# Optimization experiments

Hardware: AMD Instinct MI355X
Metric: run time of the kernel (lower is better)

Reference implementation:

```python
import jax, jax.numpy as jnp
import numpy as np

BN_EPS = 1e-5


def conv3x3(x, w, b):
    # x: [B,C,H,W], w: [O,C,3,3], same padding, stride 1
    y = jax.lax.conv_general_dilated(x, w, (1, 1), ((1, 1), (1, 1)),
                                     dimension_numbers=('NCHW', 'OIHW', 'NCHW'))
    return y + b[None, :, None, None]


def bilinear_sample(x, py, px):
    # x: [B,C,H,W]; py/px: [B,K,H,W] fractional sample coords (zero outside borders)
    B, C, H, W = x.shape
    y0 = jnp.floor(py)
    x0 = jnp.floor(px)
    wy1 = py - y0  # frac weights
    wx1 = px - x0

    def corner(yc, xc, wgt):
        valid = (yc >= 0) & (yc <= H - 1) & (xc >= 0) & (xc <= W - 1)
        yi = jnp.clip(yc, 0, H - 1).astype(jnp.int32)
        xi = jnp.clip(xc, 0, W - 1).astype(jnp.int32)
        # gather per batch: [C,H,W] indexed by [K,H,W] -> [C,K,H,W]
        g = jax.vmap(lambda img, yy, xx: img[:, yy, xx])(x, yi, xi)  # [B,C,K,H,W]
        return g * jnp.where(valid, wgt, 0.0)[:, None]

    return (corner(y0, x0, (1 - wy1) * (1 - wx1))
            + corner(y0, x0 + 1, (1 - wy1) * wx1)
            + corner(y0 + 1, x0, wy1 * (1 - wx1))
            + corner(y0 + 1, x0 + 1, wy1 * wx1))  # [B,C,9,H,W]


def deform_conv(x, conv_w, off_w, off_b, mask_w, mask_b, gamma, beta):
    B, C, H, W = x.shape
    O = conv_w.shape[0]
    offset = conv3x3(x, off_w, off_b)                      # [B,18,H,W]
    mask = jax.nn.sigmoid(conv3x3(x, mask_w, mask_b))      # [B,9,H,W]
    off = offset.reshape(B, 9, 2, H, W)                    # tap k = kh*3+kw, (dy,dx)
    ky = jnp.repeat(jnp.arange(3), 3).astype(x.dtype)      # kernel row per tap
    kx = jnp.tile(jnp.arange(3), 3).astype(x.dtype)        # kernel col per tap
    gy = jnp.arange(H, dtype=x.dtype)
    gx = jnp.arange(W, dtype=x.dtype)
    # sample position = out pos - pad + kernel idx + learned offset
    py = off[:, :, 0] + gy[None, None, :, None] + (ky - 1.0)[None, :, None, None]
    px = off[:, :, 1] + gx[None, None, None, :] + (kx - 1.0)[None, :, None, None]
    val = bilinear_sample(x, py, px)                       # [B,C,9,H,W]
    val = val * mask[:, None]                              # modulated (DCNv2)
    out = jnp.einsum('bckhw,ock->bohw', val, conv_w.reshape(O, C, 9))
    # BatchNorm (training-mode batch stats) + ReLU
    mean = out.mean(axis=(0, 2, 3))
    var = out.var(axis=(0, 2, 3))
    out = (out - mean[None, :, None, None]) * jax.lax.rsqrt(var + BN_EPS)[None, :, None, None]
    out = out * gamma[None, :, None, None] + beta[None, :, None, None]
    return jax.nn.relu(out)


def setup_inputs() -> dict:
    key = jax.random.key(0)
    ks = jax.random.split(key, 8)
    B, Cin, Cout, H, W = 2, 64, 64, 128, 128
    x = jax.random.normal(ks[0], (B, Cin, H, W), dtype=jnp.float32)
    fan = Cin * 9
    conv_w = jax.random.normal(ks[1], (Cout, Cin, 3, 3), dtype=jnp.float32) / np.sqrt(fan)
    # offset/mask convs: small random weights so offsets are non-degenerate but modest
    off_w = jax.random.normal(ks[2], (18, Cin, 3, 3), dtype=jnp.float32) * 0.01
    off_b = jax.random.normal(ks[3], (18,), dtype=jnp.float32) * 0.1
    mask_w = jax.random.normal(ks[4], (9, Cin, 3, 3), dtype=jnp.float32) * 0.01
    mask_b = jnp.zeros((9,), dtype=jnp.float32)
    gamma = jnp.ones((Cout,), dtype=jnp.float32)
    beta = jnp.zeros((Cout,), dtype=jnp.float32)
    return {"x": x, "conv_w": conv_w, "off_w": off_w, "off_b": off_b,
            "mask_w": mask_w, "mask_b": mask_b, "gamma": gamma, "beta": beta}


def reference(x, conv_w, off_w, off_b, mask_w, mask_b, gamma, beta):
    return deform_conv(x, conv_w, off_w, off_b, mask_w, mask_b, gamma, beta)
```

## Files before the change

### kernel.cpp

```cpp
#include <hip/hip_runtime.h>
#include <hip/hip_fp16.h>

typedef __attribute__((ext_vector_type(8))) _Float16 f16x8;
typedef __attribute__((ext_vector_type(4))) float f32x4;
typedef __attribute__((ext_vector_type(4))) unsigned int u32x4;
typedef unsigned int  u32;
typedef unsigned short u16;

constexpr int B_  = 2;
constexpr int C_  = 64;
constexpr int O_  = 64;
constexpr int H_  = 128;
constexpr int W_  = 128;
constexpr int HW_ = H_ * W_;
constexpr int NPIX_ = B_ * HW_;
constexpr float BN_EPS_ = 1e-5f;

constexpr int WROWS_ = 7;
constexpr int WCOLS_ = 70;
constexpr int WPIX_  = WROWS_ * WCOLS_;
constexpr int WSTR_  = 72;

__device__ __align__(16) u16   g_xt[(size_t)B_ * HW_ * 64];
__device__ __align__(16) u16   g_pre16[(size_t)B_ * O_ * HW_];
__device__ __align__(16) u16   g_WpF[36864];
__device__ __align__(16) u16   g_W27F[18432];
__device__ __align__(16) float g_part[262144];
__device__ __align__(16) float g_stats[128];

__device__ __forceinline__ u32 segsw(u32 px) { return ((px >> 3) & 3u) << 3; }

__device__ __forceinline__ u16 f2bf(float f) {
    u32 u = __float_as_uint(f);
    u = (u + 0x7fffu + ((u >> 16) & 1u)) >> 16;
    return (u16)u;
}
__device__ __forceinline__ float bflo(u32 u) { return __uint_as_float(u << 16); }
__device__ __forceinline__ float bfhi(u32 u) { return __uint_as_float(u & 0xffff0000u); }
__device__ __forceinline__ u16 f2h(float f) { return __half_as_ushort(__float2half(f)); }

__global__ __launch_bounds__(256)
void prep_kernel(const float* __restrict__ x, const float* __restrict__ conv_w,
                 const float* __restrict__ off_w, const float* __restrict__ mask_w) {
    int bid = blockIdx.x, tid = threadIdx.x;
    if (bid < 512) {
        __shared__ u16 tile[64][66];
        int b = bid >> 8;
        int hw0 = (bid & 255) * 64;
        int c = tid >> 2, pq = (tid & 3) * 16;
        const float* src = x + (((size_t)(b * 64 + c)) << 14) + hw0 + pq;
#pragma unroll
        for (int i = 0; i < 4; i++) {
            float4 v = *(const float4*)(src + i * 4);
            tile[pq + i * 4 + 0][c] = f2h(v.x);
            tile[pq + i * 4 + 1][c] = f2h(v.y);
            tile[pq + i * 4 + 2][c] = f2h(v.z);
            tile[pq + i * 4 + 3][c] = f2h(v.w);
        }
        __syncthreads();
        int p = tid >> 2, cs = (tid & 3) * 16;
        uint4* dst = (uint4*)(g_xt + (((size_t)(b << 14)) + hw0 + p) * 64 + cs);
        dst[0] = *(const uint4*)&tile[p][cs];
        dst[1] = *(const uint4*)&tile[p][cs + 8];
    } else if (bid < 512 + 144) {
        int i = (bid - 512) * 256 + tid;
        int j = i & 7, lane = (i >> 3) & 63, t = (i >> 9) & 3, s = i >> 11;
        int o = t * 16 + (lane & 15);
        int kk = s * 32 + (lane >> 4) * 8 + j;
        int tap = kk >> 6, c = kk & 63;
        g_WpF[i] = f2h(conv_w[(o * 64 + c) * 9 + tap]);
    } else {
        int i = (bid - 656) * 256 + tid;
        int j = i & 7, lane = (i >> 3) & 63, t = (i >> 9) & 1, s = i >> 10;
        int row = t * 16 + (lane & 15);
        int kk = s * 32 + (lane >> 4) * 8 + j;
        int tap = kk >> 6, c = kk & 63;
        float v = 0.f;
        if (row < 18) v = off_w[(row * 64 + c) * 9 + tap];
        else if (row < 27) v = mask_w[((row - 18) * 64 + c) * 9 + tap];
        g_W27F[i] = f2h(v);
    }
}

__device__ __forceinline__ void mfma4h(int lane, int sg, const f16x8& sv,
                                       f32x4 (&acc)[4]) {
#pragma unroll
    for (int t = 0; t < 4; t++) {
        f16x8 af = *(const f16x8*)(g_WpF + (u32)((sg * 4 + t) * 64 + lane) * 8u);
        acc[t] = __builtin_amdgcn_mfma_f32_16x16x32_f16(af, sv, acc[t], 0, 0, 0);
    }
}

__device__ __forceinline__ void metaBrt(const float* __restrict__ moff,
                                        const float* __restrict__ mmask,
                                        int tap, int p64, int h, int w, int cb,
                                        u32 qoff, u32* qc, u32* cwp) {
    float dy = moff[(2 * tap) * 64 + p64];
    float dx = moff[(2 * tap + 1) * 64 + p64];
    float m  = mmask[tap * 64 + p64];
    float kdy = (float)(tap / 3 - 1), kdx = (float)(tap % 3 - 1);
    float py = dy + (float)h + kdy;
    float px = dx + (float)w + kdx;
    float y0 = floorf(py), x0 = floorf(px);
    float ly = py - y0, lx = px - x0, hy = 1.f - ly, hx = 1.f - lx;
    float y1 = y0 + 1.f, x1 = x0 + 1.f;
    bool vy0 = (y0 >= 0.f) && (y0 <= 127.f);
    bool vy1 = (y1 >= 0.f) && (y1 <= 127.f);
    bool vx0 = (x0 >= 0.f) && (x0 <= 127.f);
    bool vx1 = (x1 >= 0.f) && (x1 <= 127.f);
    int iy0 = (int)fminf(fmaxf(y0, 0.f), 127.f);
    int iy1 = (int)fminf(fmaxf(y1, 0.f), 127.f);
    int ix0 = (int)fminf(fmaxf(x0, 0.f), 127.f);
    int ix1 = (int)fminf(fmaxf(x1, 0.f), 127.f);
    int w00 = min(max(iy0 * WCOLS_ + ix0 - cb, 0), WPIX_ - 1);
    int w01 = min(max(iy0 * WCOLS_ + ix1 - cb, 0), WPIX_ - 1);
    int w10 = min(max(iy1 * WCOLS_ + ix0 - cb, 0), WPIX_ - 1);
    int w11 = min(max(iy1 * WCOLS_ + ix1 - cb, 0), WPIX_ - 1);
    qc[0] = (u32)w00 * WSTR_ + (qoff ^ segsw((u32)w00));
    qc[1] = (u32)w01 * WSTR_ + (qoff ^ segsw((u32)w01));
    qc[2] = (u32)w10 * WSTR_ + (qoff ^ segsw((u32)w10));
    qc[3] = (u32)w11 * WSTR_ + (qoff ^ segsw((u32)w11));
    __half2 c0 = __float2half2_rn((vy0 && vx0) ? hy * hx * m : 0.f);
    __half2 c1 = __float2half2_rn((vy0 && vx1) ? hy * lx * m : 0.f);
    __half2 c2 = __float2half2_rn((vy1 && vx0) ? ly * hx * m : 0.f);
    __half2 c3 = __float2half2_rn((vy1 && vx1) ? ly * lx * m : 0.f);
    cwp[0] = *(const u32*)&c0; cwp[1] = *(const u32*)&c1;
    cwp[2] = *(const u32*)&c2; cwp[3] = *(const u32*)&c3;
}

__device__ __forceinline__ void ld4(const u16* __restrict__ win, const u32* qc,
                                    u32 sc, uint4* p) {
#pragma unroll
    for (int i = 0; i < 4; i++) p[i] = *(const uint4*)(win + qc[i] + sc);
}

__device__ __forceinline__ f16x8 cmbH(const uint4* p, const u32* cwp) {
    const u32* a = &p[0].x; const u32* b = &p[1].x;
    const u32* c = &p[2].x; const u32* d = &p[3].x;
    __half2 cw0 = *(const __half2*)&cwp[0], cw1 = *(const __half2*)&cwp[1];
    __half2 cw2 = *(const __half2*)&cwp[2], cw3 = *(const __half2*)&cwp[3];
    u32x4 r;
#pragma unroll
    for (int i = 0; i < 4; i++) {
        __half2 t = __hmul2(*(const __half2*)&a[i], cw0);
        t = __hfma2(*(const __half2*)&b[i], cw1, t);
        t = __hfma2(*(const __half2*)&c[i], cw2, t);
        t = __hfma2(*(const __half2*)&d[i], cw3, t);
        r[i] = *(const u32*)&t;
    }
    return __builtin_bit_cast(f16x8, r);
}

template<int OS>
__device__ __forceinline__ void phaseB(const u16* __restrict__ win,
                                       const float* __restrict__ moff,
                                       const float* __restrict__ mmask,
                                       int p64, int h, int w, int cb,
                                       u32 qoff, int lane, f32x4 (&acc)[4]) {
    u32 q[4]; u32 cw[4];
#pragma unroll
    for (int ls = 0; ls < 9; ls++) {
        const int s   = OS * 9 + ls;
        const int tap = s >> 1;
        const int kh  = s & 1;
        if (kh == 0 || ls == 0)
            metaBrt(moff, mmask, tap, p64, h, w, cb, qoff, q, cw);
        uint4 p[4];
        ld4(win, q, (u32)(kh * 32), p);
        f16x8 sv = cmbH(p, cw);
        mfma4h(lane, s, sv, acc);
    }
}

__global__ __launch_bounds__(512, 4)
void gemm_ab_kernel(const float* __restrict__ off_b, const float* __restrict__ mask_b) {
    __shared__ __align__(16) u16 win[(WPIX_ + 1) * WSTR_];
    __shared__ float moff[18 * 64];
    __shared__ float mmask[9 * 64];
    const int tid = threadIdx.x;
    const int lane = tid & 63, wv = tid >> 6;
    const int quad = lane >> 4, r = lane & 15;
    const int wp = wv & 3, os = wv >> 2;
    const int blk = (blockIdx.x & 7) * 64 + (blockIdx.x >> 3);
    const int pbase = blk * 64;
    const int b = pbase >> 14, hwb = pbase & (HW_ - 1);
    const int h = hwb >> 7, w0 = hwb & (W_ - 1);
    const int p64 = wp * 16 + r;
    const int w = w0 + p64;
    const int cb = (h - 3) * WCOLS_ + (w0 - 3);
    const u32 bb = (u32)b << 14;
    const u32 qoff = (u32)quad * 8u;

#pragma unroll
    for (int it = 0; it < 8; it++) {
        int i = tid + it * 512;
        if (i < WPIX_ * 8) {
            int px = i >> 3, seg = i & 7;
            int wr = px / WCOLS_, wc = px - wr * WCOLS_;
            int row = min(max(h - 3 + wr, 0), H_ - 1);
            int col = min(max(w0 - 3 + wc, 0), W_ - 1);
            u32 g = (bb + (u32)(row * W_ + col)) * 64u + (u32)seg * 8u;
            u32 d = (u32)px * WSTR_ + (((u32)seg * 8u) ^ segsw((u32)px));
            *(uint4*)(&win[d]) = *(const uint4*)(g_xt + g);
        } else if (i < WPIX_ * 8 + 8) {
            int seg = i - WPIX_ * 8;
            u32 d = (u32)WPIX_ * WSTR_ + (((u32)seg * 8u) ^ segsw((u32)WPIX_));
            *(uint4*)(&win[d]) = make_uint4(0, 0, 0, 0);
        }
    }
    __syncthreads();

    {
        u32 aq[9];
#pragma unroll
        for (int tap = 0; tap < 9; tap++) {
            int dh = tap / 3 - 1, dw = tap % 3 - 1;
            int hh = h + dh, ww = w + dw;
            bool valid = (hh >= 0) && (hh < H_) && (ww >= 0) && (ww < W_);
            u32 widx = valid ? (u32)((3 + dh) * WCOLS_ + (p64 + 3 + dw)) : (u32)WPIX_;
            aq[tap] = widx * WSTR_ + (qoff ^ segsw(widx));
        }
        f32x4 accA = (f32x4){0.f, 0.f, 0.f, 0.f};
        f16x8 ab[3];
        ab[0] = *(const f16x8*)(win + aq[0]);
        ab[1] = *(const f16x8*)(win + aq[0] + 32);
        ab[2] = *(const f16x8*)(win + aq[1]);
#pragma unroll
        for (int s = 0; s < 18; s++) {
            f16x8 sv = ab[s % 3];
            if (s + 3 < 18)
                ab[s % 3] = *(const f16x8*)(win + aq[(s + 3) >> 1] + ((s + 3) & 1) * 32);
            f16x8 af = *(const f16x8*)(g_W27F + (u32)((s * 2 + os) * 64 + lane) * 8u);
            accA = __builtin_amdgcn_mfma_f32_16x16x32_f16(af, sv, accA, 0, 0, 0);
        }
#pragma unroll
        for (int g = 0; g < 4; g++) {
            int o = os * 16 + quad * 4 + g;
            float v = accA[g];
            if (o < 18) {
                moff[o * 64 + p64] = v + off_b[o];
            } else if (o < 27) {
                v += mask_b[o - 18];
                mmask[(o - 18) * 64 + p64] = 1.f / (1.f + __expf(-v));
            }
        }
    }
    __syncthreads();

    f32x4 acc[4];
#pragma unroll
    for (int t = 0; t < 4; t++) acc[t] = (f32x4){0.f, 0.f, 0.f, 0.f};

    if (os == 0)
        phaseB<0>(win, moff, mmask, p64, h, w, cb, qoff, lane, acc);
    else
        phaseB<1>(win, moff, mmask, p64, h, w, cb, qoff, lane, acc);
    __syncthreads();

    float* ex = (float*)win;
    const u32 exi = (u32)p64 * 68u + (((u32)quad << 2) ^ ((((u32)p64 >> 3) & 3u) << 2));
    if (os == 1) {
#pragma unroll
        for (int t = 0; t < 4; t++)
            *(f32x4*)(ex + exi + (u32)t * 16u) = acc[t];
    }
    __syncthreads();

    if (os == 0) {
#pragma unroll
        for (int t = 0; t < 4; t++)
            acc[t] += *(const f32x4*)(ex + exi + (u32)t * 16u);

        const int hw = hwb + p64;
        const u32 slot = (u32)(blk * 4 + wp);
#pragma unroll
        for (int t = 0; t < 4; t++) {
#pragma unroll
            for (int g = 0; g < 4; g++) {
                float v = acc[t][g];
                int o = t * 16 + quad * 4 + g;
                g_pre16[(u32)(b * 64 + o) * HW_ + hw] = f2bf(v);
                float s = v, s2 = v * v;
#pragma unroll
                for (int off = 8; off >= 1; off >>= 1) {
                    s  += __shfl_down(s, off, 16);
                    s2 += __shfl_down(s2, off, 16);
                }
                if (r == 0) {
                    g_part[(u32)o * 2048 + slot] = s;
                    g_part[131072 + (u32)o * 2048 + slot] = s2;
                }
            }
        }
    }
}

__global__ __launch_bounds__(256)
void stats_red_kernel() {
    __shared__ float p4[4];
    int i = blockIdx.x;
    const float* src = g_part + (u32)(i >> 6) * 131072 + (u32)(i & 63) * 2048;
    float s = 0.f;
    for (int rr = threadIdx.x; rr < 2048; rr += 256) s += src[rr];
#pragma unroll
    for (int off = 32; off >= 1; off >>= 1) s += __shfl_down(s, off);
    if ((threadIdx.x & 63) == 0) p4[threadIdx.x >> 6] = s;
    __syncthreads();
    if (threadIdx.x == 0) g_stats[i] = p4[0] + p4[1] + p4[2] + p4[3];
}

__global__ __launch_bounds__(256)
void bn_relu_kernel(const float* __restrict__ gamma, const float* __restrict__ beta,
                    float* __restrict__ out) {
    int i4 = blockIdx.x * 256 + threadIdx.x;
    int ch = (i4 >> 12) & (O_ - 1);
    float mean = g_stats[ch] * (1.f / NPIX_);
    float var  = g_stats[64 + ch] * (1.f / NPIX_) - mean * mean;
    float scale = gamma[ch] * rsqrtf(var + BN_EPS_);
    float shift = beta[ch] - mean * scale;
    uint2 v = ((const uint2*)g_pre16)[i4];
    float4 o;
    o.x = fmaxf(fmaf(bflo(v.x), scale, shift), 0.f);
    o.y = fmaxf(fmaf(bfhi(v.x), scale, shift), 0.f);
    o.z = fmaxf(fmaf(bflo(v.y), scale, shift), 0.f);
    o.w = fmaxf(fmaf(bfhi(v.y), scale, shift), 0.f);
    ((float4*)out)[i4] = o;
}

extern "C" void kernel_launch(void* const* d_in, const int* in_sizes, int n_in,
                              void* d_out, int out_size, void* d_ws, size_t ws_size,
                              hipStream_t stream) {
    const float* x      = (const float*)d_in[0];
    const float* conv_w = (const float*)d_in[1];
    const float* off_w  = (const float*)d_in[2];
    const float* off_b  = (const float*)d_in[3];
    const float* mask_w = (const float*)d_in[4];
    const float* mask_b = (const float*)d_in[5];
    const float* gamma  = (const float*)d_in[6];
    const float* beta   = (const float*)d_in[7];
    float* out = (float*)d_out;
    (void)d_ws; (void)ws_size;

    prep_kernel<<<728, 256, 0, stream>>>(x, conv_w, off_w, mask_w);
    gemm_ab_kernel<<<NPIX_ / 64, 512, 0, stream>>>(off_b, mask_b);
    stats_red_kernel<<<128, 256, 0, stream>>>();
    bn_relu_kernel<<<2048, 256, 0, stream>>>(gamma, beta, out);
}
```

Baseline: 98.58 us.

## Read input directly from global memory instead of staging LDS window, halve block size

Removes the shared-memory halo window of channel-last input and has both the offset/mask conv and the bilinear gathers read g_xt directly from global (L1/L2), using a zero pixel appended at the end for padding. It also drops the two-wave-group split over taps and the LDS cross-group reduction, so each wave handles all 18 K-steps with 256 threads per block. This removes the window fill, several barriers and LDS pressure, which should allow more resident blocks. In exchange, the gathers become scattered global loads with cache-dependent latency, and each wave does twice the serial MFMA work.

```diff
diff --git a/kernel.cpp b/kernel.cpp
--- a/kernel.cpp
+++ b/kernel.cpp
@@ -16,19 +16,12 @@
 constexpr int NPIX_ = B_ * HW_;
 constexpr float BN_EPS_ = 1e-5f;
 
-constexpr int WROWS_ = 7;
-constexpr int WCOLS_ = 70;
-constexpr int WPIX_  = WROWS_ * WCOLS_;
-constexpr int WSTR_  = 72;
-
-__device__ __align__(16) u16   g_xt[(size_t)B_ * HW_ * 64];
+__device__ __align__(16) u16   g_xt[((size_t)NPIX_ + 1) * 64];
 __device__ __align__(16) u16   g_pre16[(size_t)B_ * O_ * HW_];
 __device__ __align__(16) u16   g_WpF[36864];
 __device__ __align__(16) u16   g_W27F[18432];
 __device__ __align__(16) float g_part[262144];
 __device__ __align__(16) float g_stats[128];
-
-__device__ __forceinline__ u32 segsw(u32 px) { return ((px >> 3) & 3u) << 3; }
 
 __device__ __forceinline__ u16 f2bf(float f) {
     u32 u = __float_as_uint(f);
@@ -79,6 +72,7 @@
         if (row < 18) v = off_w[(row * 64 + c) * 9 + tap];
         else if (row < 27) v = mask_w[((row - 18) * 64 + c) * 9 + tap];
         g_W27F[i] = f2h(v);
+        if (bid == 656 && tid < 64) g_xt[(size_t)NPIX_ * 64 + tid] = 0;
     }
 }
 
@@ -91,10 +85,10 @@
     }
 }
 
-__device__ __forceinline__ void metaBrt(const float* __restrict__ moff,
-                                        const float* __restrict__ mmask,
-                                        int tap, int p64, int h, int w, int cb,
-                                        u32 qoff, u32* qc, u32* cwp) {
+__device__ __forceinline__ void metaBrtG(const float* __restrict__ moff,
+                                         const float* __restrict__ mmask,
+                                         int tap, int p64, int h, int w, u32 bb,
+                                         u32 qoff, u32* qc, u32* cwp) {
     float dy = moff[(2 * tap) * 64 + p64];
     float dx = moff[(2 * tap + 1) * 64 + p64];
     float m  = mmask[tap * 64 + p64];
@@ -112,14 +106,10 @@
     int iy1 = (int)fminf(fmaxf(y1, 0.f), 127.f);
     int ix0 = (int)fminf(fmaxf(x0, 0.f), 127.f);
     int ix1 = (int)fminf(fmaxf(x1, 0.f), 127.f);
-    int w00 = min(max(iy0 * WCOLS_ + ix0 - cb, 0), WPIX_ - 1);
-    int w01 = min(max(iy0 * WCOLS_ + ix1 - cb, 0), WPIX_ - 1);
-    int w10 = min(max(iy1 * WCOLS_ + ix0 - cb, 0), WPIX_ - 1);
-    int w11 = min(max(iy1 * WCOLS_ + ix1 - cb, 0), WPIX_ - 1);
-    qc[0] = (u32)w00 * WSTR_ + (qoff ^ segsw((u32)w00));
-    qc[1] = (u32)w01 * WSTR_ + (qoff ^ segsw((u32)w01));
-    qc[2] = (u32)w10 * WSTR_ + (qoff ^ segsw((u32)w10));
-    qc[3] = (u32)w11 * WSTR_ + (qoff ^ segsw((u32)w11));
+    qc[0] = (bb + (u32)(iy0 * W_ + ix0)) * 64u + qoff;
+    qc[1] = (bb + (u32)(iy0 * W_ + ix1)) * 64u + qoff;
+    qc[2] = (bb + (u32)(iy1 * W_ + ix0)) * 64u + qoff;
+    qc[3] = (bb + (u32)(iy1 * W_ + ix1)) * 64u + qoff;
     __half2 c0 = __float2half2_rn((vy0 && vx0) ? hy * hx * m : 0.f);
     __half2 c1 = __float2half2_rn((vy0 && vx1) ? hy * lx * m : 0.f);
     __half2 c2 = __float2half2_rn((vy1 && vx0) ? ly * hx * m : 0.f);
@@ -128,10 +118,9 @@
     cwp[2] = *(const u32*)&c2; cwp[3] = *(const u32*)&c3;
 }
 
-__device__ __forceinline__ void ld4(const u16* __restrict__ win, const u32* qc,
-                                    u32 sc, uint4* p) {
-#pragma unroll
-    for (int i = 0; i < 4; i++) p[i] = *(const uint4*)(win + qc[i] + sc);
+__device__ __forceinline__ void ld4g(const u32* qc, u32 sc, uint4* p) {
+#pragma unroll
+    for (int i = 0; i < 4; i++) p[i] = *(const uint4*)(g_xt + qc[i] + sc);
 }
 
 __device__ __forceinline__ f16x8 cmbH(const uint4* p, const u32* cwp) {
@@ -151,64 +140,21 @@
     return __builtin_bit_cast(f16x8, r);
 }
 
-template<int OS>
-__device__ __forceinline__ void phaseB(const u16* __restrict__ win,
-                                       const float* __restrict__ moff,
-                                       const float* __restrict__ mmask,
-                                       int p64, int h, int w, int cb,
-                                       u32 qoff, int lane, f32x4 (&acc)[4]) {
-    u32 q[4]; u32 cw[4];
-#pragma unroll
-    for (int ls = 0; ls < 9; ls++) {
-        const int s   = OS * 9 + ls;
-        const int tap = s >> 1;
-        const int kh  = s & 1;
-        if (kh == 0 || ls == 0)
-            metaBrt(moff, mmask, tap, p64, h, w, cb, qoff, q, cw);
-        uint4 p[4];
-        ld4(win, q, (u32)(kh * 32), p);
-        f16x8 sv = cmbH(p, cw);
-        mfma4h(lane, s, sv, acc);
-    }
-}
-
-__global__ __launch_bounds__(512, 4)
+__global__ __launch_bounds__(256, 4)
 void gemm_ab_kernel(const float* __restrict__ off_b, const float* __restrict__ mask_b) {
-    __shared__ __align__(16) u16 win[(WPIX_ + 1) * WSTR_];
     __shared__ float moff[18 * 64];
     __shared__ float mmask[9 * 64];
     const int tid = threadIdx.x;
     const int lane = tid & 63, wv = tid >> 6;
     const int quad = lane >> 4, r = lane & 15;
-    const int wp = wv & 3, os = wv >> 2;
     const int blk = (blockIdx.x & 7) * 64 + (blockIdx.x >> 3);
     const int pbase = blk * 64;
     const int b = pbase >> 14, hwb = pbase & (HW_ - 1);
     const int h = hwb >> 7, w0 = hwb & (W_ - 1);
-    const int p64 = wp * 16 + r;
+    const int p64 = wv * 16 + r;
     const int w = w0 + p64;
-    const int cb = (h - 3) * WCOLS_ + (w0 - 3);
     const u32 bb = (u32)b << 14;
     const u32 qoff = (u32)quad * 8u;
-
-#pragma unroll
-    for (int it = 0; it < 8; it++) {
-        int i = tid + it * 512;
-        if (i < WPIX_ * 8) {
-            int px = i >> 3, seg = i & 7;
-            int wr = px / WCOLS_, wc = px - wr * WCOLS_;
-            int row = min(max(h - 3 + wr, 0), H_ - 1);
-            int col = min(max(w0 - 3 + wc, 0), W_ - 1);
-            u32 g = (bb + (u32)(row * W_ + col)) * 64u + (u32)seg * 8u;
-            u32 d = (u32)px * WSTR_ + (((u32)seg * 8u) ^ segsw((u32)px));
-            *(uint4*)(&win[d]) = *(const uint4*)(g_xt + g);
-        } else if (i < WPIX_ * 8 + 8) {
-            int seg = i - WPIX_ * 8;
-            u32 d = (u32)WPIX_ * WSTR_ + (((u32)seg * 8u) ^ segsw((u32)WPIX_));
-            *(uint4*)(&win[d]) = make_uint4(0, 0, 0, 0);
-        }
-    }
-    __syncthreads();
 
     {
         u32 aq[9];
@@ -217,79 +163,84 @@
             int dh = tap / 3 - 1, dw = tap % 3 - 1;
             int hh = h + dh, ww = w + dw;
             bool valid = (hh >= 0) && (hh < H_) && (ww >= 0) && (ww < W_);
-            u32 widx = valid ? (u32)((3 + dh) * WCOLS_ + (p64 + 3 + dw)) : (u32)WPIX_;
-            aq[tap] = widx * WSTR_ + (qoff ^ segsw(widx));
-        }
-        f32x4 accA = (f32x4){0.f, 0.f, 0.f, 0.f};
+            u32 pix = valid ? (bb + (u32)(hh * W_ + ww)) : (u32)NPIX_;
+            aq[tap] = pix * 64u + qoff;
+        }
+        f32x4 accA[2];
+        accA[0] = (f32x4){0.f, 0.f, 0.f, 0.f};
+        accA[1] = (f32x4){0.f, 0.f, 0.f, 0.f};
         f16x8 ab[3];
-        ab[0] = *(const f16x8*)(win + aq[0]);
-        ab[1] = *(const f16x8*)(win + aq[0] + 32);
-        ab[2] = *(const f16x8*)(win + aq[1]);
+        ab[0] = *(const f16x8*)(g_xt + aq[0]);
+        ab[1] = *(const f16x8*)(g_xt + aq[0] + 32);
+        ab[2] = *(const f16x8*)(g_xt + aq[1]);
 #pragma unroll
         for (int s = 0; s < 18; s++) {
             f16x8 sv = ab[s % 3];
             if (s + 3 < 18)
-                ab[s % 3] = *(const f16x8*)(win + aq[(s + 3) >> 1] + ((s + 3) & 1) * 32);
-            f16x8 af = *(const f16x8*)(g_W27F + (u32)((s * 2 + os) * 64 + lane) * 8u);
-            accA = __builtin_amdgcn_mfma_f32_16x16x32_f16(af, sv, accA, 0, 0, 0);
-        }
+                ab[s % 3] = *(const f16x8*)(g_xt + aq[(s + 3) >> 1] + ((s + 3) & 1) * 32);
+#pragma unroll
+            for (int t = 0; t < 2; t++) {
+                f16x8 af = *(const f16x8*)(g_W27F + (u32)((s * 2 + t) * 64 + lane) * 8u);
+                accA[t] = __builtin_amdgcn_mfma_f32_16x16x32_f16(af, sv, accA[t], 0, 0, 0);
+            }
+        }
+#pragma unroll
+        for (int t = 0; t < 2; t++) {
+#pragma unroll
+            for (int g = 0; g < 4; g++) {
+                int o = t * 16 + quad * 4 + g;
+                float v = accA[t][g];
+                if (o < 18) {
+                    moff[o * 64 + p64] = v + off_b[o];
+                } else if (o < 27) {
+                    v += mask_b[o - 18];
+                    mmask[(o - 18) * 64 + p64] = 1.f / (1.f + __expf(-v));
+                }
+            }
+        }
+    }
+
+    f32x4 acc[4];
+#pragma unroll
+    for (int t = 0; t < 4; t++) acc[t] = (f32x4){0.f, 0.f, 0.f, 0.f};
+    {
+        u32 q[4]; u32 cw[4];
+#pragma unroll
+        for (int tap = 0; tap < 9; tap++) {
+            metaBrtG(moff, mmask, tap, p64, h, w, bb, qoff, q, cw);
+            {
+                uint4 p0[4];
+                ld4g(q, 0, p0);
+                f16x8 sv = cmbH(p0, cw);
+                mfma4h(lane, tap * 2 + 0, sv, acc);
+            }
+            {
+                uint4 p1[4];
+                ld4g(q, 32, p1);
+                f16x8 sv = cmbH(p1, cw);
+                mfma4h(lane, tap * 2 + 1, sv, acc);
+            }
+        }
+    }
+
+    const int hw = hwb + p64;
+    const u32 slot = (u32)(blk * 4 + wv);
+#pragma unroll
+    for (int t = 0; t < 4; t++) {
 #pragma unroll
         for (int g = 0; g < 4; g++) {
-            int o = os * 16 + quad * 4 + g;
-            float v = accA[g];
-            if (o < 18) {
-                moff[o * 64 + p64] = v + off_b[o];
-            } else if (o < 27) {
-                v += mask_b[o - 18];
-                mmask[(o - 18) * 64 + p64] = 1.f / (1.f + __expf(-v));
-            }
-        }
-    }
-    __syncthreads();
-
-    f32x4 acc[4];
-#pragma unroll
-    for (int t = 0; t < 4; t++) acc[t] = (f32x4){0.f, 0.f, 0.f, 0.f};
-
-    if (os == 0)
-        phaseB<0>(win, moff, mmask, p64, h, w, cb, qoff, lane, acc);
-    else
-        phaseB<1>(win, moff, mmask, p64, h, w, cb, qoff, lane, acc);
-    __syncthreads();
-
-    float* ex = (float*)win;
-    const u32 exi = (u32)p64 * 68u + (((u32)quad << 2) ^ ((((u32)p64 >> 3) & 3u) << 2));
-    if (os == 1) {
-#pragma unroll
-        for (int t = 0; t < 4; t++)
-            *(f32x4*)(ex + exi + (u32)t * 16u) = acc[t];
-    }
-    __syncthreads();
-
-    if (os == 0) {
-#pragma unroll
-        for (int t = 0; t < 4; t++)
-            acc[t] += *(const f32x4*)(ex + exi + (u32)t * 16u);
-
-        const int hw = hwb + p64;
-        const u32 slot = (u32)(blk * 4 + wp);
-#pragma unroll
-        for (int t = 0; t < 4; t++) {
-#pragma unroll
-            for (int g = 0; g < 4; g++) {
-                float v = acc[t][g];
-                int o = t * 16 + quad * 4 + g;
-                g_pre16[(u32)(b * 64 + o) * HW_ + hw] = f2bf(v);
-                float s = v, s2 = v * v;
-#pragma unroll
-                for (int off = 8; off >= 1; off >>= 1) {
-                    s  += __shfl_down(s, off, 16);
-                    s2 += __shfl_down(s2, off, 16);
-                }
-                if (r == 0) {
-                    g_part[(u32)o * 2048 + slot] = s;
-                    g_part[131072 + (u32)o * 2048 + slot] = s2;
-                }
+            float v = acc[t][g];
+            int o = t * 16 + quad * 4 + g;
+            g_pre16[(u32)(b * 64 + o) * HW_ + hw] = f2bf(v);
+            float s = v, s2 = v * v;
+#pragma unroll
+            for (int off = 8; off >= 1; off >>= 1) {
+                s  += __shfl_down(s, off, 16);
+                s2 += __shfl_down(s2, off, 16);
+            }
+            if (r == 0) {
+                g_part[(u32)o * 2048 + slot] = s;
+                g_part[131072 + (u32)o * 2048 + slot] = s2;
             }
         }
     }
@@ -342,7 +293,7 @@
     (void)d_ws; (void)ws_size;
 
     prep_kernel<<<728, 256, 0, stream>>>(x, conv_w, off_w, mask_w);
-    gemm_ab_kernel<<<NPIX_ / 64, 512, 0, stream>>>(off_b, mask_b);
+    gemm_ab_kernel<<<NPIX_ / 64, 256, 0, stream>>>(off_b, mask_b);
     stats_red_kernel<<<128, 256, 0, stream>>>();
     bn_relu_kernel<<<2048, 256, 0, stream>>>(gamma, beta, out);
 }
```

After: 113.3 us. 1.15x slower.
